# Optimization experiments

Hardware: AMD Instinct MI355X
Metric: run time of the kernel (lower is better)

Reference implementation:

```python
import jax, jax.numpy as jnp
import numpy as np

N_NODES = 50000


def spmm(rows, cols, vals, dense):
    # out[i,:] = sum_{e: rows[e]==i} vals[e] * dense[cols[e], :]
    gathered = dense[cols] * vals[:, None]  # [E, D]
    return jax.ops.segment_sum(gathered, rows, num_segments=N_NODES)


def setup_inputs() -> dict:
    key = jax.random.key(0)
    k1, k2, k3, k4, k5, k6 = jax.random.split(key, 6)
    N, E, F, H, C = N_NODES, 800000, 512, 256, 64
    node_features = jax.random.normal(k1, (N, F), dtype=jnp.float32)
    adj_rows = jax.random.randint(k2, (E,), 0, N, dtype=jnp.int32)
    adj_cols = jax.random.randint(k3, (E,), 0, N, dtype=jnp.int32)
    adj_vals = jax.random.uniform(k4, (E,), dtype=jnp.float32)
    W1 = jax.random.normal(k5, (F, H), dtype=jnp.float32) * (1.0 / np.sqrt(F))
    b1 = jnp.zeros((H,), dtype=jnp.float32)
    W2 = jax.random.normal(k6, (H, C), dtype=jnp.float32) * (1.0 / np.sqrt(H))
    b2 = jnp.zeros((C,), dtype=jnp.float32)
    return {"node_features": node_features, "adj_rows": adj_rows,
            "adj_cols": adj_cols, "adj_vals": adj_vals,
            "W1": W1, "b1": b1, "W2": W2, "b2": b2}


def reference(node_features, adj_rows, adj_cols, adj_vals, W1, b1, W2, b2):
    # Layer 1: dense projection then sparse aggregation, then ReLU.
    support1 = node_features @ W1 + b1           # [N, H]
    x = jax.nn.relu(spmm(adj_rows, adj_cols, adj_vals, support1))
    # Dropout is identity in eval mode (training=False).
    # Layer 2
    support2 = x @ W2 + b2                       # [N, C]
    x = spmm(adj_rows, adj_cols, adj_vals, support2)
    return jax.nn.log_softmax(x, axis=1)
```

## Files before the change

kernel.cpp:

```cpp
#include <hip/hip_runtime.h>

#define N_NODES 50000
#define N_EDGES 800000
#define F_IN    512
#define H_DIM   256
#define C_DIM   64
#define MPAD    50048

#define NB      196
#define NCHUNK  49
#define CHUNK   16384
#define BCAP    6144

typedef __bf16 bf16;
typedef __bf16 bf16x4 __attribute__((ext_vector_type(4)));
typedef __bf16 bf16x8 __attribute__((ext_vector_type(8)));
typedef float  f32x4  __attribute__((ext_vector_type(4)));
typedef unsigned int u32;
typedef unsigned char u8;

__device__ __forceinline__ void gl_lds16(const void* g, void* l) {
    __builtin_amdgcn_global_load_lds(
        (const __attribute__((address_space(1))) u32*)g,
        (__attribute__((address_space(3))) u32*)l, 16, 0, 0);
}

__device__ __forceinline__ float unpack_val(u32 pk) {
    return __builtin_bit_cast(float, pk << 16);
}


__global__ __launch_bounds__(1024) void histA_k(const int* __restrict__ rows,
                                                u32* __restrict__ G) {
    __shared__ u32 h[16 * NB];
    int tid = threadIdx.x, wid = tid >> 6;
    for (int i = tid; i < 16 * NB; i += 1024) h[i] = 0;
    __syncthreads();
    int base = blockIdx.x * CHUNK;
    int end = base + CHUNK; if (end > N_EDGES) end = N_EDGES;
    for (int e = base + tid; e < end; e += 1024)
        atomicAdd(&h[wid * NB + (rows[e] >> 8)], 1);
    __syncthreads();
    if (tid < NB) {
        u32 s = 0;
#pragma unroll
        for (int w = 0; w < 16; w++) s += h[w * NB + tid];
        G[tid * NCHUNK + blockIdx.x] = s;
    }
}

__global__ __launch_bounds__(1024) void scatterB_k(const int* __restrict__ rows,
                                                   const int* __restrict__ cols,
                                                   const float* __restrict__ vals,
                                                   const u32* __restrict__ G,
                                                   u32* __restrict__ epack,
                                                   u8* __restrict__ lrow) {
    __shared__ u32 cur[NB];
    __shared__ u32 wtot[16];
    int tid = threadIdx.x, wid = tid >> 6, lane = tid & 63;
    int c = blockIdx.x;
    u32 tot = 0, pre = 0;
    if (tid < NB) {
        for (int cc = 0; cc < NCHUNK; cc++) {
            u32 v = G[tid * NCHUNK + cc];
            tot += v;
            if (cc < c) pre += v;
        }
    }
    u32 incl = tot;
#pragma unroll
    for (int off = 1; off < 64; off <<= 1) {
        u32 u = __shfl_up(incl, off, 64);
        if (lane >= off) incl += u;
    }
    if (lane == 63) wtot[wid] = incl;
    __syncthreads();
    u32 wpre = 0;
#pragma unroll
    for (int w = 0; w < 16; w++)
        if (w < wid) wpre += wtot[w];
    if (tid < NB) cur[tid] = (wpre + incl - tot) + pre;
    __syncthreads();
    int base = c * CHUNK;
    int end = base + CHUNK; if (end > N_EDGES) end = N_EDGES;
    for (int e = base + tid; e < end; e += 1024) {
        int r = rows[e];
        unsigned short vb = __builtin_bit_cast(unsigned short, (bf16)vals[e]);
        u32 pk = ((u32)cols[e] << 16) | (u32)vb;
        u32 p = atomicAdd(&cur[r >> 8], 1);
        epack[p] = pk;
        lrow[p] = (u8)(r & 255);
    }
}

__global__ __launch_bounds__(256) void sortC_k(u32* __restrict__ epack,
                                               const u8* __restrict__ lrow,
                                               const u32* __restrict__ G,
                                               int* __restrict__ starts) {
    __shared__ u32 edat[BCAP];
    __shared__ u32 sdat[BCAP];
    __shared__ u8  erow[BCAP];
    __shared__ u32 h[4 * 256];
    __shared__ u32 cur[256];
    __shared__ u32 wt1[4], wt2[4];
    __shared__ u32 sh_s, sh_n;
    int b = blockIdx.x, tid = threadIdx.x, wid = tid >> 6, lane = tid & 63;

    u32 btot = 0;
    if (tid < NB)
        for (int cc = 0; cc < NCHUNK; cc++) btot += G[tid * NCHUNK + cc];
    u32 bincl = btot;
#pragma unroll
    for (int off = 1; off < 64; off <<= 1) {
        u32 u = __shfl_up(bincl, off, 64);
        if (lane >= off) bincl += u;
    }
    if (lane == 63) wt1[wid] = bincl;
    __syncthreads();
    u32 bwpre = 0;
#pragma unroll
    for (int w = 0; w < 4; w++)
        if (w < wid) bwpre += wt1[w];
    if (tid == b) { sh_s = bwpre + bincl - btot; sh_n = btot; }
    __syncthreads();
    int s = (int)sh_s;
    int n = (int)sh_n;
    if (n > BCAP) n = BCAP;

    for (int i = tid; i < n; i += 256) { edat[i] = epack[s + i]; erow[i] = lrow[s + i]; }
    for (int i = tid; i < 1024; i += 256) h[i] = 0;
    __syncthreads();
    for (int i = tid; i < n; i += 256) atomicAdd(&h[wid * 256 + erow[i]], 1);
    __syncthreads();
    u32 tot = h[tid] + h[256 + tid] + h[512 + tid] + h[768 + tid];
    u32 incl = tot;
#pragma unroll
    for (int off = 1; off < 64; off <<= 1) {
        u32 u = __shfl_up(incl, off, 64);
        if (lane >= off) incl += u;
    }
    if (lane == 63) wt2[wid] = incl;
    __syncthreads();
    u32 wpre = 0;
#pragma unroll
    for (int w = 0; w < 4; w++)
        if (w < wid) wpre += wt2[w];
    u32 excl = wpre + incl - tot;
    cur[tid] = excl;
    int grow = b * 256 + tid;
    if (grow < N_NODES) starts[grow] = s + (int)excl;
    if (b == 0 && tid == 0) starts[N_NODES] = N_EDGES;
    __syncthreads();
    for (int i = tid; i < n; i += 256) {
        u32 p = atomicAdd(&cur[erow[i]], 1);
        sdat[p] = edat[i];
    }
    __syncthreads();
    for (int i = tid; i < n; i += 256) epack[s + i] = sdat[i];
}


__global__ __launch_bounds__(256) void tr_w_k(const float* __restrict__ W1,
                                              const float* __restrict__ W2,
                                              bf16* __restrict__ W1t,
                                              bf16* __restrict__ W2t) {
    int i = blockIdx.x * 256 + threadIdx.x;
    if (i < F_IN * H_DIM) {
        int k = i >> 8, n = i & 255;
        W1t[n * F_IN + k] = (bf16)W1[i];
    } else {
        int j = i - F_IN * H_DIM;
        int k = j >> 6, n = j & 63;
        W2t[n * H_DIM + k] = (bf16)W2[j];
    }
}


__global__ __launch_bounds__(512) void gemm1_k(const float* __restrict__ A,
                                               const bf16* __restrict__ Bt,
                                               const float* __restrict__ bias,
                                               bf16* __restrict__ C) {
    constexpr int BM = 128, BN = 256, BK = 64;
    __shared__ bf16 As[BM * BK];
    __shared__ bf16 Bs[BN * BK];

    int tid = threadIdx.x;
    int wid = tid >> 6, lane = tid & 63;
    int wr = wid >> 2, wc = wid & 3;
    int bm = blockIdx.x;

    f32x4 acc[4][4];
#pragma unroll
    for (int m = 0; m < 4; m++)
#pragma unroll
        for (int n = 0; n < 4; n++) acc[m][n] = (f32x4){0.f, 0.f, 0.f, 0.f};

    for (int kt = 0; kt < F_IN; kt += BK) {
#pragma unroll
        for (int j = 0; j < 4; j++) {
            int ch = j * 512 + tid;
            int row = ch >> 3, kc = ch & 7;
            gl_lds16(Bt + (size_t)row * F_IN + kt + kc * 8,
                     &Bs[(j * 512 + wid * 64) * 8]);
        }
#pragma unroll
        for (int j = 0; j < 2; j++) {
            int ch = j * 512 + tid;
            int row = ch >> 3, kc = ch & 7;
            int ar = bm * BM + row;
            if (ar >= N_NODES) ar = N_NODES - 1;
            const f32x4* src = (const f32x4*)(A + (size_t)ar * F_IN + kt + kc * 8);
            f32x4 u = src[0], v = src[1];
            bf16x8 o;
            o[0] = (bf16)u[0]; o[1] = (bf16)u[1]; o[2] = (bf16)u[2]; o[3] = (bf16)u[3];
            o[4] = (bf16)v[0]; o[5] = (bf16)v[1]; o[6] = (bf16)v[2]; o[7] = (bf16)v[3];
            *(bf16x8*)&As[(size_t)ch * 8] = o;
        }
        __syncthreads();

        bf16x8 afr[2][4], bfr[2][4];
#pragma unroll
        for (int kk = 0; kk < 2; kk++) {
#pragma unroll
            for (int m = 0; m < 4; m++)
                afr[kk][m] = *(const bf16x8*)&As[(wr * 64 + m * 16 + (lane & 15)) * BK +
                                                 kk * 32 + (lane >> 4) * 8];
#pragma unroll
            for (int n = 0; n < 4; n++)
                bfr[kk][n] = *(const bf16x8*)&Bs[(wc * 64 + n * 16 + (lane & 15)) * BK +
                                                 kk * 32 + (lane >> 4) * 8];
        }
#pragma unroll
        for (int kk = 0; kk < 2; kk++)
#pragma unroll
            for (int m = 0; m < 4; m++)
#pragma unroll
                for (int n = 0; n < 4; n++)
                    acc[m][n] = __builtin_amdgcn_mfma_f32_16x16x32_bf16(
                        afr[kk][m], bfr[kk][n], acc[m][n], 0, 0, 0);
        __syncthreads();
    }

#pragma unroll
    for (int m = 0; m < 4; m++) {
        int row0 = bm * BM + wr * 64 + m * 16 + (lane >> 4) * 4;
#pragma unroll
        for (int n = 0; n < 4; n++) {
            int col = wc * 64 + n * 16 + (lane & 15);
            float bz = bias[col];
#pragma unroll
            for (int r = 0; r < 4; r++) {
                int row = row0 + r;
                if (row < N_NODES)
                    C[(size_t)row * H_DIM + col] = (bf16)(acc[m][n][r] + bz);
            }
        }
    }
}


__global__ __launch_bounds__(256) void gemm2_k(const bf16* __restrict__ A,
                                               const bf16* __restrict__ Bt,
                                               const float* __restrict__ bias,
                                               bf16* __restrict__ C) {
    constexpr int BM = 128, BK = 64;
    __shared__ bf16 As[BM * BK];
    __shared__ bf16 Bs[64 * BK];

    int tid = threadIdx.x;
    int wid = tid >> 6, lane = tid & 63;
    int wr = wid >> 1, wc = wid & 1;
    int bm = blockIdx.x;

    f32x4 acc[4][2];
#pragma unroll
    for (int m = 0; m < 4; m++)
#pragma unroll
        for (int n = 0; n < 2; n++) acc[m][n] = (f32x4){0.f, 0.f, 0.f, 0.f};

    for (int kt = 0; kt < H_DIM; kt += BK) {
#pragma unroll
        for (int j = 0; j < 4; j++) {
            int ch = j * 256 + tid;
            int row = ch >> 3, kc = ch & 7;
            gl_lds16(A + (size_t)(bm * BM + row) * H_DIM + kt + kc * 8,
                     &As[(j * 256 + wid * 64) * 8]);
        }
#pragma unroll
        for (int j = 0; j < 2; j++) {
            int ch = j * 256 + tid;
            int row = ch >> 3, kc = ch & 7;
            gl_lds16(Bt + (size_t)row * H_DIM + kt + kc * 8,
                     &Bs[(j * 256 + wid * 64) * 8]);
        }
        __syncthreads();

        bf16x8 afr[2][4], bfr[2][2];
#pragma unroll
        for (int kk = 0; kk < 2; kk++) {
#pragma unroll
            for (int m = 0; m < 4; m++)
                afr[kk][m] = *(const bf16x8*)&As[(wr * 64 + m * 16 + (lane & 15)) * BK +
                                                 kk * 32 + (lane >> 4) * 8];
#pragma unroll
            for (int n = 0; n < 2; n++)
                bfr[kk][n] = *(const bf16x8*)&Bs[(wc * 32 + n * 16 + (lane & 15)) * BK +
                                                 kk * 32 + (lane >> 4) * 8];
        }
#pragma unroll
        for (int kk = 0; kk < 2; kk++)
#pragma unroll
            for (int m = 0; m < 4; m++)
#pragma unroll
                for (int n = 0; n < 2; n++)
                    acc[m][n] = __builtin_amdgcn_mfma_f32_16x16x32_bf16(
                        afr[kk][m], bfr[kk][n], acc[m][n], 0, 0, 0);
        __syncthreads();
    }

#pragma unroll
    for (int m = 0; m < 4; m++) {
        int row0 = bm * BM + wr * 64 + m * 16 + (lane >> 4) * 4;
#pragma unroll
        for (int n = 0; n < 2; n++) {
            int col = wc * 32 + n * 16 + (lane & 15);
            float bz = bias[col];
#pragma unroll
            for (int r = 0; r < 4; r++) {
                int row = row0 + r;
                if (row < N_NODES)
                    C[(size_t)row * C_DIM + col] = (bf16)(acc[m][n][r] + bz);
            }
        }
    }
}


__global__ __launch_bounds__(256) void spmm1_k(const int* __restrict__ starts,
                                               const u32* __restrict__ epack,
                                               const bf16* __restrict__ s1,
                                               bf16* __restrict__ x16) {
    int wid = threadIdx.x >> 6, lane = threadIdx.x & 63;
    int row = blockIdx.x * 4 + wid;
    if (row >= N_NODES) return;
    int s = starts[row], e = starts[row + 1];
    f32x4 acc = (f32x4){0.f, 0.f, 0.f, 0.f};
    const bf16* s1l = s1 + lane * 4;
    int p = s;
    for (; p + 8 <= e; p += 8) {
        u32 k0 = epack[p],     k1 = epack[p + 1], k2 = epack[p + 2], k3 = epack[p + 3];
        u32 k4 = epack[p + 4], k5 = epack[p + 5], k6 = epack[p + 6], k7 = epack[p + 7];
        bf16x4 g0 = *(const bf16x4*)(s1l + (size_t)(k0 >> 16) * H_DIM);
        bf16x4 g1 = *(const bf16x4*)(s1l + (size_t)(k1 >> 16) * H_DIM);
        bf16x4 g2 = *(const bf16x4*)(s1l + (size_t)(k2 >> 16) * H_DIM);
        bf16x4 g3 = *(const bf16x4*)(s1l + (size_t)(k3 >> 16) * H_DIM);
        bf16x4 g4 = *(const bf16x4*)(s1l + (size_t)(k4 >> 16) * H_DIM);
        bf16x4 g5 = *(const bf16x4*)(s1l + (size_t)(k5 >> 16) * H_DIM);
        bf16x4 g6 = *(const bf16x4*)(s1l + (size_t)(k6 >> 16) * H_DIM);
        bf16x4 g7 = *(const bf16x4*)(s1l + (size_t)(k7 >> 16) * H_DIM);
        float v0 = unpack_val(k0), v1 = unpack_val(k1), v2 = unpack_val(k2), v3 = unpack_val(k3);
        float v4 = unpack_val(k4), v5 = unpack_val(k5), v6 = unpack_val(k6), v7 = unpack_val(k7);
#pragma unroll
        for (int j = 0; j < 4; j++)
            acc[j] += v0 * (float)g0[j] + v1 * (float)g1[j] +
                      v2 * (float)g2[j] + v3 * (float)g3[j] +
                      v4 * (float)g4[j] + v5 * (float)g5[j] +
                      v6 * (float)g6[j] + v7 * (float)g7[j];
    }
    for (; p < e; ++p) {
        u32 k = epack[p];
        float v = unpack_val(k);
        bf16x4 g = *(const bf16x4*)(s1l + (size_t)(k >> 16) * H_DIM);
#pragma unroll
        for (int j = 0; j < 4; j++) acc[j] += v * (float)g[j];
    }
    bf16x4 o;
#pragma unroll
    for (int j = 0; j < 4; j++) o[j] = (bf16)fmaxf(acc[j], 0.f);
    *(bf16x4*)(x16 + (size_t)row * H_DIM + lane * 4) = o;
}


__global__ __launch_bounds__(256) void spmm2_sm_k(const int* __restrict__ starts,
                                                  const u32* __restrict__ epack,
                                                  const bf16* __restrict__ s2,
                                                  float* __restrict__ out) {
    int wid = threadIdx.x >> 6, lane = threadIdx.x & 63;
    int row = blockIdx.x * 4 + wid;
    if (row >= N_NODES) return;
    int s = starts[row], e = starts[row + 1];
    float acc = 0.f;
    int p = s;
    for (; p + 8 <= e; p += 8) {
        u32 k0 = epack[p],     k1 = epack[p + 1], k2 = epack[p + 2], k3 = epack[p + 3];
        u32 k4 = epack[p + 4], k5 = epack[p + 5], k6 = epack[p + 6], k7 = epack[p + 7];
        float g0 = (float)s2[(size_t)(k0 >> 16) * C_DIM + lane];
        float g1 = (float)s2[(size_t)(k1 >> 16) * C_DIM + lane];
        float g2 = (float)s2[(size_t)(k2 >> 16) * C_DIM + lane];
        float g3 = (float)s2[(size_t)(k3 >> 16) * C_DIM + lane];
        float g4 = (float)s2[(size_t)(k4 >> 16) * C_DIM + lane];
        float g5 = (float)s2[(size_t)(k5 >> 16) * C_DIM + lane];
        float g6 = (float)s2[(size_t)(k6 >> 16) * C_DIM + lane];
        float g7 = (float)s2[(size_t)(k7 >> 16) * C_DIM + lane];
        acc += unpack_val(k0) * g0 + unpack_val(k1) * g1 +
               unpack_val(k2) * g2 + unpack_val(k3) * g3 +
               unpack_val(k4) * g4 + unpack_val(k5) * g5 +
               unpack_val(k6) * g6 + unpack_val(k7) * g7;
    }
    for (; p < e; ++p) {
        u32 k = epack[p];
        acc += unpack_val(k) * (float)s2[(size_t)(k >> 16) * C_DIM + lane];
    }
    float mx = acc;
#pragma unroll
    for (int off = 32; off >= 1; off >>= 1) mx = fmaxf(mx, __shfl_xor(mx, off, 64));
    float ex = expf(acc - mx);
    float se = ex;
#pragma unroll
    for (int off = 32; off >= 1; off >>= 1) se += __shfl_xor(se, off, 64);
    out[(size_t)row * C_DIM + lane] = (acc - mx) - logf(se);
}


extern "C" void kernel_launch(void* const* d_in, const int* in_sizes, int n_in,
                              void* d_out, int out_size, void* d_ws, size_t ws_size,
                              hipStream_t stream) {
    const float* nf   = (const float*)d_in[0];
    const int*   rows = (const int*)d_in[1];
    const int*   cols = (const int*)d_in[2];
    const float* vals = (const float*)d_in[3];
    const float* W1   = (const float*)d_in[4];
    const float* b1   = (const float*)d_in[5];
    const float* W2   = (const float*)d_in[6];
    const float* b2   = (const float*)d_in[7];
    float* out = (float*)d_out;

    char* w = (char*)d_ws;
    auto alloc = [&](size_t b) { void* p = (void*)w; w += (b + 255) & ~(size_t)255; return p; };

    bf16* x16  = (bf16*)alloc((size_t)MPAD * H_DIM * 2);
    bf16* sup1 = (bf16*)alloc((size_t)N_NODES * H_DIM * 2);
    bf16* sup2 = sup1;
    bf16* W1t = (bf16*)alloc((size_t)H_DIM * F_IN * 2);
    bf16* W2t = (bf16*)alloc((size_t)C_DIM * H_DIM * 2);
    int* starts = (int*)alloc((size_t)(N_NODES + 1) * 4);
    u32* G      = (u32*)alloc((size_t)NB * NCHUNK * 4);
    u32* epack  = (u32*)alloc((size_t)N_EDGES * 4);
    u8*  lrow   = (u8*)alloc((size_t)N_EDGES);

    histA_k<<<NCHUNK, 1024, 0, stream>>>(rows, G);
    scatterB_k<<<NCHUNK, 1024, 0, stream>>>(rows, cols, vals, G, epack, lrow);
    sortC_k<<<NB, 256, 0, stream>>>(epack, lrow, G, starts);

    tr_w_k<<<(F_IN * H_DIM + H_DIM * C_DIM) / 256, 256, 0, stream>>>(W1, W2, W1t, W2t);

    gemm1_k<<<MPAD / 128, 512, 0, stream>>>(nf, W1t, b1, sup1);
    spmm1_k<<<(N_NODES + 3) / 4, 256, 0, stream>>>(starts, epack, sup1, x16);

    gemm2_k<<<MPAD / 128, 256, 0, stream>>>(x16, W2t, b2, sup2);
    spmm2_sm_k<<<(N_NODES + 3) / 4, 256, 0, stream>>>(starts, epack, sup2, out);

    (void)in_sizes; (void)n_in; (void)out_size; (void)ws_size;
}
```

Baseline: 190.7 us.

## Fuse histogram with weight transpose, shrink GEMM1 tile, use nontemporal edge loads

```diff
diff --git a/kernel.cpp b/kernel.cpp
--- a/kernel.cpp
+++ b/kernel.cpp
@@ -17,6 +17,7 @@
 typedef __bf16 bf16x8 __attribute__((ext_vector_type(8)));
 typedef float  f32x4  __attribute__((ext_vector_type(4)));
 typedef unsigned int u32;
+typedef unsigned long long u64;
 typedef unsigned char u8;
 
 __device__ __forceinline__ void gl_lds16(const void* g, void* l) {
@@ -30,24 +31,44 @@
 }
 
 
-__global__ __launch_bounds__(1024) void histA_k(const int* __restrict__ rows,
-                                                u32* __restrict__ G) {
+__global__ __launch_bounds__(1024) void prep_k(const int* __restrict__ rows,
+                                               const float* __restrict__ W1,
+                                               const float* __restrict__ W2,
+                                               u32* __restrict__ G,
+                                               bf16* __restrict__ W1t,
+                                               bf16* __restrict__ W2t) {
     __shared__ u32 h[16 * NB];
-    int tid = threadIdx.x, wid = tid >> 6;
-    for (int i = tid; i < 16 * NB; i += 1024) h[i] = 0;
-    __syncthreads();
-    int base = blockIdx.x * CHUNK;
-    int end = base + CHUNK; if (end > N_EDGES) end = N_EDGES;
-    for (int e = base + tid; e < end; e += 1024)
-        atomicAdd(&h[wid * NB + (rows[e] >> 8)], 1);
-    __syncthreads();
-    if (tid < NB) {
-        u32 s = 0;
-#pragma unroll
-        for (int w = 0; w < 16; w++) s += h[w * NB + tid];
-        G[tid * NCHUNK + blockIdx.x] = s;
-    }
-}
+    int bid = blockIdx.x, tid = threadIdx.x;
+    if (bid < NCHUNK) {
+        int wid = tid >> 6;
+        for (int i = tid; i < 16 * NB; i += 1024) h[i] = 0;
+        __syncthreads();
+        int base = bid * CHUNK;
+        int end = base + CHUNK; if (end > N_EDGES) end = N_EDGES;
+        for (int e = base + tid; e < end; e += 1024)
+            atomicAdd(&h[wid * NB + (rows[e] >> 8)], 1);
+        __syncthreads();
+        if (tid < NB) {
+            u32 s = 0;
+#pragma unroll
+            for (int w = 0; w < 16; w++) s += h[w * NB + tid];
+            G[tid * NCHUNK + bid] = s;
+        }
+    } else {
+        int i = (bid - NCHUNK) * 1024 + tid;
+        if (i < F_IN * H_DIM) {
+            int k = i >> 8, n = i & 255;
+            W1t[n * F_IN + k] = (bf16)W1[i];
+        } else {
+            int j = i - F_IN * H_DIM;
+            if (j < H_DIM * C_DIM) {
+                int k = j >> 6, n = j & 63;
+                W2t[n * H_DIM + k] = (bf16)W2[j];
+            }
+        }
+    }
+}
+
 
 __global__ __launch_bounds__(1024) void scatterB_k(const int* __restrict__ rows,
                                                    const int* __restrict__ cols,
@@ -93,6 +114,7 @@
     }
 }
 
+
 __global__ __launch_bounds__(256) void sortC_k(u32* __restrict__ epack,
                                                const u8* __restrict__ lrow,
                                                const u32* __restrict__ G,
@@ -160,33 +182,16 @@
 }
 
 
-__global__ __launch_bounds__(256) void tr_w_k(const float* __restrict__ W1,
-                                              const float* __restrict__ W2,
-                                              bf16* __restrict__ W1t,
-                                              bf16* __restrict__ W2t) {
-    int i = blockIdx.x * 256 + threadIdx.x;
-    if (i < F_IN * H_DIM) {
-        int k = i >> 8, n = i & 255;
-        W1t[n * F_IN + k] = (bf16)W1[i];
-    } else {
-        int j = i - F_IN * H_DIM;
-        int k = j >> 6, n = j & 63;
-        W2t[n * H_DIM + k] = (bf16)W2[j];
-    }
-}
-
-
-__global__ __launch_bounds__(512) void gemm1_k(const float* __restrict__ A,
+__global__ __launch_bounds__(256) void gemm1_k(const float* __restrict__ A,
                                                const bf16* __restrict__ Bt,
                                                const float* __restrict__ bias,
                                                bf16* __restrict__ C) {
-    constexpr int BM = 128, BN = 256, BK = 64;
+    constexpr int BM = 64, BK = 64;
     __shared__ bf16 As[BM * BK];
-    __shared__ bf16 Bs[BN * BK];
+    __shared__ bf16 Bs[256 * BK];
 
     int tid = threadIdx.x;
     int wid = tid >> 6, lane = tid & 63;
-    int wr = wid >> 2, wc = wid & 3;
     int bm = blockIdx.x;
 
     f32x4 acc[4][4];
@@ -197,15 +202,15 @@
 
     for (int kt = 0; kt < F_IN; kt += BK) {
 #pragma unroll
-        for (int j = 0; j < 4; j++) {
-            int ch = j * 512 + tid;
+        for (int j = 0; j < 8; j++) {
+            int ch = j * 256 + tid;
             int row = ch >> 3, kc = ch & 7;
             gl_lds16(Bt + (size_t)row * F_IN + kt + kc * 8,
-                     &Bs[(j * 512 + wid * 64) * 8]);
+                     &Bs[(j * 256 + wid * 64) * 8]);
         }
 #pragma unroll
         for (int j = 0; j < 2; j++) {
-            int ch = j * 512 + tid;
+            int ch = j * 256 + tid;
             int row = ch >> 3, kc = ch & 7;
             int ar = bm * BM + row;
             if (ar >= N_NODES) ar = N_NODES - 1;
@@ -223,11 +228,11 @@
         for (int kk = 0; kk < 2; kk++) {
 #pragma unroll
             for (int m = 0; m < 4; m++)
-                afr[kk][m] = *(const bf16x8*)&As[(wr * 64 + m * 16 + (lane & 15)) * BK +
+                afr[kk][m] = *(const bf16x8*)&As[(m * 16 + (lane & 15)) * BK +
                                                  kk * 32 + (lane >> 4) * 8];
 #pragma unroll
             for (int n = 0; n < 4; n++)
-                bfr[kk][n] = *(const bf16x8*)&Bs[(wc * 64 + n * 16 + (lane & 15)) * BK +
+                bfr[kk][n] = *(const bf16x8*)&Bs[(wid * 64 + n * 16 + (lane & 15)) * BK +
                                                  kk * 32 + (lane >> 4) * 8];
         }
 #pragma unroll
@@ -243,10 +248,10 @@
 
 #pragma unroll
     for (int m = 0; m < 4; m++) {
-        int row0 = bm * BM + wr * 64 + m * 16 + (lane >> 4) * 4;
+        int row0 = bm * BM + m * 16 + (lane >> 4) * 4;
 #pragma unroll
         for (int n = 0; n < 4; n++) {
-            int col = wc * 64 + n * 16 + (lane & 15);
+            int col = wid * 64 + n * 16 + (lane & 15);
             float bz = bias[col];
 #pragma unroll
             for (int r = 0; r < 4; r++) {
@@ -348,8 +353,14 @@
     const bf16* s1l = s1 + lane * 4;
     int p = s;
     for (; p + 8 <= e; p += 8) {
-        u32 k0 = epack[p],     k1 = epack[p + 1], k2 = epack[p + 2], k3 = epack[p + 3];
-        u32 k4 = epack[p + 4], k5 = epack[p + 5], k6 = epack[p + 6], k7 = epack[p + 7];
+        u32 k0 = __builtin_nontemporal_load(epack + p);
+        u32 k1 = __builtin_nontemporal_load(epack + p + 1);
+        u32 k2 = __builtin_nontemporal_load(epack + p + 2);
+        u32 k3 = __builtin_nontemporal_load(epack + p + 3);
+        u32 k4 = __builtin_nontemporal_load(epack + p + 4);
+        u32 k5 = __builtin_nontemporal_load(epack + p + 5);
+        u32 k6 = __builtin_nontemporal_load(epack + p + 6);
+        u32 k7 = __builtin_nontemporal_load(epack + p + 7);
         bf16x4 g0 = *(const bf16x4*)(s1l + (size_t)(k0 >> 16) * H_DIM);
         bf16x4 g1 = *(const bf16x4*)(s1l + (size_t)(k1 >> 16) * H_DIM);
         bf16x4 g2 = *(const bf16x4*)(s1l + (size_t)(k2 >> 16) * H_DIM);
@@ -368,7 +379,7 @@
                       v6 * (float)g6[j] + v7 * (float)g7[j];
     }
     for (; p < e; ++p) {
-        u32 k = epack[p];
+        u32 k = __builtin_nontemporal_load(epack + p);
         float v = unpack_val(k);
         bf16x4 g = *(const bf16x4*)(s1l + (size_t)(k >> 16) * H_DIM);
 #pragma unroll
@@ -377,7 +388,8 @@
     bf16x4 o;
 #pragma unroll
     for (int j = 0; j < 4; j++) o[j] = (bf16)fmaxf(acc[j], 0.f);
-    *(bf16x4*)(x16 + (size_t)row * H_DIM + lane * 4) = o;
+    u64 bits = __builtin_bit_cast(u64, o);
+    __builtin_nontemporal_store(bits, (u64*)(x16 + (size_t)row * H_DIM + lane * 4));
 }
 
 
@@ -392,8 +404,14 @@
     float acc = 0.f;
     int p = s;
     for (; p + 8 <= e; p += 8) {
-        u32 k0 = epack[p],     k1 = epack[p + 1], k2 = epack[p + 2], k3 = epack[p + 3];
-        u32 k4 = epack[p + 4], k5 = epack[p + 5], k6 = epack[p + 6], k7 = epack[p + 7];
+        u32 k0 = __builtin_nontemporal_load(epack + p);
+        u32 k1 = __builtin_nontemporal_load(epack + p + 1);
+        u32 k2 = __builtin_nontemporal_load(epack + p + 2);
+        u32 k3 = __builtin_nontemporal_load(epack + p + 3);
+        u32 k4 = __builtin_nontemporal_load(epack + p + 4);
+        u32 k5 = __builtin_nontemporal_load(epack + p + 5);
+        u32 k6 = __builtin_nontemporal_load(epack + p + 6);
+        u32 k7 = __builtin_nontemporal_load(epack + p + 7);
         float g0 = (float)s2[(size_t)(k0 >> 16) * C_DIM + lane];
         float g1 = (float)s2[(size_t)(k1 >> 16) * C_DIM + lane];
         float g2 = (float)s2[(size_t)(k2 >> 16) * C_DIM + lane];
@@ -408,7 +426,7 @@
                unpack_val(k6) * g6 + unpack_val(k7) * g7;
     }
     for (; p < e; ++p) {
-        u32 k = epack[p];
+        u32 k = __builtin_nontemporal_load(epack + p);
         acc += unpack_val(k) * (float)s2[(size_t)(k >> 16) * C_DIM + lane];
     }
     float mx = acc;
@@ -418,7 +436,8 @@
     float se = ex;
 #pragma unroll
     for (int off = 32; off >= 1; off >>= 1) se += __shfl_xor(se, off, 64);
-    out[(size_t)row * C_DIM + lane] = (acc - mx) - logf(se);
+    __builtin_nontemporal_store((acc - mx) - logf(se),
+                                out + (size_t)row * C_DIM + lane);
 }
 
 
@@ -448,15 +467,11 @@
     u32* epack  = (u32*)alloc((size_t)N_EDGES * 4);
     u8*  lrow   = (u8*)alloc((size_t)N_EDGES);
 
-    histA_k<<<NCHUNK, 1024, 0, stream>>>(rows, G);
+    prep_k<<<NCHUNK + 144, 1024, 0, stream>>>(rows, W1, W2, G, W1t, W2t);
     scatterB_k<<<NCHUNK, 1024, 0, stream>>>(rows, cols, vals, G, epack, lrow);
     sortC_k<<<NB, 256, 0, stream>>>(epack, lrow, G, starts);
-
-    tr_w_k<<<(F_IN * H_DIM + H_DIM * C_DIM) / 256, 256, 0, stream>>>(W1, W2, W1t, W2t);
-
-    gemm1_k<<<MPAD / 128, 512, 0, stream>>>(nf, W1t, b1, sup1);
+    gemm1_k<<<MPAD / 64, 256, 0, stream>>>(nf, W1t, b1, sup1);
     spmm1_k<<<(N_NODES + 3) / 4, 256, 0, stream>>>(starts, epack, sup1, x16);
-
     gemm2_k<<<MPAD / 128, 256, 0, stream>>>(x16, W2t, b2, sup2);
     spmm2_sm_k<<<(N_NODES + 3) / 4, 256, 0, stream>>>(starts, epack, sup2, out);
 
```

Result: slower. 215.3 us (+12.9%).
